# Kernel optimization log

Hardware: AMD Instinct MI355X
Metric: run time of the kernel (lower is better)

The kernel has to match this reference:

```python
import jax, jax.numpy as jnp
import numpy as np
import math

DIM = 1024
D_IN = 2048      # expand * dim
N = 16           # d_state
NG = 32          # ngroups
DT_RANK = 64     # ceil(dim/16)
D_CONV = 4
B, L = 2, 1024


def setup_inputs() -> dict:
    key = jax.random.key(0)
    ks = jax.random.split(key, 10)
    nrm = lambda k, shp, s: jax.random.normal(k, shp, jnp.float32) * s
    x = jax.random.normal(ks[0], (B, L, DIM), jnp.float32)
    latent = jnp.zeros((B, NG, D_IN, N), jnp.float32)
    W_in = nrm(ks[1], (2 * D_IN, DIM), 0.02)          # in_proj (no bias)
    conv_w = nrm(ks[2], (D_IN, 1, D_CONV), 0.1)        # depthwise conv weight
    conv_b = nrm(ks[3], (D_IN,), 0.02)                 # conv bias
    W_x = nrm(ks[4], (DT_RANK + 2 * N, D_IN), 0.02)    # x_proj (no bias)
    W_dt = nrm(ks[5], (D_IN, DT_RANK), 0.02)           # dt_proj weight
    b_dt = nrm(ks[6], (D_IN,), 0.1)                    # dt_proj bias
    W_out = nrm(ks[7], (DIM, D_IN), 0.02)              # out_proj (no bias)
    A_log = jnp.log(jnp.tile(jnp.arange(1, N + 1, dtype=jnp.float32), (D_IN, 1)))
    D = jnp.ones((D_IN,), jnp.float32)
    W_cattn = nrm(ks[8], (3 * N, N), 0.02)             # c_attn (no bias)
    return dict(x=x, latent=latent, W_in=W_in, conv_w=conv_w, conv_b=conv_b,
                W_x=W_x, W_dt=W_dt, b_dt=b_dt, W_out=W_out, A_log=A_log,
                D=D, W_cattn=W_cattn)


def _scan_op(e1, e2):
    a1, b1 = e1
    a2, b2 = e2
    return a2 * a1, a2 * b1 + b2


def reference(x, latent, W_in, conv_w, conv_b, W_x, W_dt, b_dt, W_out, A_log, D, W_cattn):
    b, l, _ = x.shape
    xr = x @ W_in.T                                  # [b,l,2*d_in]
    u, res = xr[..., :D_IN], xr[..., D_IN:]
    # depthwise causal conv1d (padding d_conv-1 then truncate to l == left-pad)
    uc = jnp.transpose(u, (0, 2, 1))                 # [b,d_in,l]
    uc = jax.lax.conv_general_dilated(
        uc, conv_w, window_strides=(1,), padding=[(D_CONV - 1, 0)],
        feature_group_count=D_IN, dimension_numbers=('NCH', 'OIH', 'NCH'))
    uc = uc + conv_b[None, :, None]
    u = jax.nn.silu(jnp.transpose(uc, (0, 2, 1)))    # [b,l,d_in]

    A = -jnp.exp(A_log)                              # [d_in,n]
    x_dbl = u @ W_x.T                                # [b,l,dt_rank+2n]
    delta = jax.nn.softplus(x_dbl[..., :DT_RANK] @ W_dt.T + b_dt)  # [b,l,d_in]
    Bm = x_dbl[..., DT_RANK:DT_RANK + N]             # [b,l,n]
    Cm = x_dbl[..., DT_RANK + N:]                    # [b,l,n]

    dA = jnp.exp(delta[..., None] * A)               # [b,l,d_in,n]
    dBu = delta[..., None] * Bm[:, :, None, :] * u[..., None]  # [b,l,d_in,n]

    pg = l // NG
    dA = dA.reshape(b, NG, pg, D_IN, N)
    dBu = dBu.reshape(b, NG, pg, D_IN, N)
    Cg = Cm.reshape(b, NG, pg, N)
    dBu = dBu.at[:, :, 0].add(latent)                # inject group latent

    # parallel scan of h_t = dA_t * h_{t-1} + dBu_t within each group
    _, hs = jax.lax.associative_scan(_scan_op, (dA, dBu), axis=2)
    y = jnp.einsum('bgpdn,bgpn->bgpd', hs, Cg).reshape(b, l, D_IN)
    y = y + u * D

    # latent communication: causal attention over group latents (initial latent, per source)
    qkv = latent[:, :-1] @ W_cattn.T                 # [b,ng-1,d_in,3n]
    q, k, v = jnp.split(qkv, 3, axis=-1)
    G = NG - 1
    q = q.reshape(b, G, -1)
    k = k.reshape(b, G, -1)
    v = v.reshape(b, G, -1)
    scale = 1.0 / math.sqrt(D_IN * N)
    scores = (q @ jnp.swapaxes(k, 1, 2)) * scale     # [b,G,G]
    mask = jnp.tril(jnp.ones((G, G), bool))
    scores = jnp.where(mask, scores, -jnp.inf)
    attn = jax.nn.softmax(scores, axis=-1)
    lat = (attn @ v).reshape(b, G, D_IN, N)
    lat_out = jnp.concatenate([jnp.zeros((b, 1, D_IN, N), x.dtype), lat], axis=1)

    out = (y * jax.nn.silu(res)) @ W_out.T           # [b,l,dim]
    return out, lat_out
```

## Files before the change

### kernel.cpp

```cpp
#include <hip/hip_runtime.h>
#include <stdint.h>

typedef uint16_t u16;
typedef u16   u16x4  __attribute__((ext_vector_type(4)));
typedef u16   u16x8  __attribute__((ext_vector_type(8)));
typedef __bf16 bf16x8 __attribute__((ext_vector_type(8)));
typedef float f32x4  __attribute__((ext_vector_type(4)));

__device__ __forceinline__ float b2f(u16 x) {
    union { uint32_t u; float f; } c; c.u = ((uint32_t)x) << 16; return c.f;
}
__device__ __forceinline__ u16 f2b(float f) {
    union { float f; uint32_t u; } c; c.f = f;
    uint32_t r = c.u + 0x7FFFu + ((c.u >> 16) & 1u);
    return (u16)(r >> 16);
}
__device__ __forceinline__ float silu_f(float x) { return x / (1.f + __expf(-x)); }

__device__ __forceinline__ void gload16(const u16* g, u16* l) {
    __builtin_amdgcn_global_load_lds(
        (const __attribute__((address_space(1))) void*)(g),
        (__attribute__((address_space(3))) void*)(l), 16, 0, 0);
}

__device__ __forceinline__ int dtype_flag_block(const u16* __restrict__ xraw) {
    __shared__ int bad;
    if (threadIdx.x == 0) bad = 0;
    __syncthreads();
    float v = b2f(xraw[threadIdx.x]);
    if (!(fabsf(v) < 1000.f)) atomicAdd(&bad, 1);
    __syncthreads();
    return bad;
}

struct CvtArgs {
    const void* s[14];
    u16* d[14];
    int cum[15];
    int total;
};
__global__ __launch_bounds__(256) void cvt_all_k(CvtArgs a, const u16* __restrict__ xraw)
{
    int flag = dtype_flag_block(xraw);
    int u4 = blockIdx.x * 256 + threadIdx.x;
    if (u4 >= a.total) return;
    int seg = 0;
    while (u4 >= a.cum[seg + 1]) seg++;
    int local = u4 - a.cum[seg];
    const void* s = a.s[seg];
    u16x4 o;
    if (s == nullptr) {
        o[0] = o[1] = o[2] = o[3] = 0;
    } else if (flag) {
        f32x4 vv = ((const f32x4*)s)[local];
        for (int e = 0; e < 4; e++) o[e] = f2b(vv[e]);
    } else {
        o = ((const u16x4*)s)[local];
    }
    *(u16x4*)(a.d[seg] + (size_t)local * 4) = o;
}

template<int EPI, int AF32>
__device__ __forceinline__ void gemm_core(
    int bx, int by, int bz,
    const u16* __restrict__ Ab, const float* __restrict__ Af,
    const u16* __restrict__ B,
    int Kc, int lda, int ldb,
    u16* __restrict__ Cb, float* __restrict__ Cf, int ldc, int ncols,
    const u16* __restrict__ bias, size_t zslab)
{
    __shared__ __align__(16) u16 lA[128 * 64];
    __shared__ __align__(16) u16 lB[128 * 64];
    const int tid  = threadIdx.x;
    const int wave = tid >> 6, lane = tid & 63;
    const int quad = lane >> 4, l16 = lane & 15;
    const int wm = wave & 1, wn = wave >> 1;
    const int row0 = by * 128, col0 = bx * 128;
    const int kbeg = bz * Kc;

    f32x4 acc[4][4];
    const f32x4 zf = {0.f, 0.f, 0.f, 0.f};
    for (int i = 0; i < 4; i++) for (int j = 0; j < 4; j++) acc[i][j] = zf;

    const u16* Abp[4]; const float* Afp[4]; const u16* Bp[4];
    int lbase[4], lofsA[4];
    for (int t = 0; t < 4; t++) {
        int c = t * 256 + tid;
        int r = c >> 3, s = c & 7;
        int q = (s - (r >> 1)) & 7;
        if (AF32) Afp[t] = Af + (size_t)(row0 + r) * lda + q * 8 + kbeg;
        else      Abp[t] = Ab + (size_t)(row0 + r) * lda + q * 8 + kbeg;
        Bp[t] = B + (size_t)(col0 + r) * ldb + q * 8 + kbeg;
        lbase[t] = (t * 256 + wave * 64) * 8;
        lofsA[t] = c * 8;
    }

    for (int k0 = 0; k0 < Kc; k0 += 64) {
        if (AF32) {
            for (int t = 0; t < 4; t++) {
                const float* ap = Afp[t] + k0;
                f32x4 v0 = *(const f32x4*)ap;
                f32x4 v1 = *(const f32x4*)(ap + 4);
                u16x8 w;
                for (int e = 0; e < 4; e++) { w[e] = f2b(v0[e]); w[4 + e] = f2b(v1[e]); }
                *(u16x8*)&lA[lofsA[t]] = w;
            }
        } else {
            for (int t = 0; t < 4; t++) gload16(Abp[t] + k0, &lA[lbase[t]]);
        }
        for (int t = 0; t < 4; t++) gload16(Bp[t] + k0, &lB[lbase[t]]);
        __syncthreads();
        for (int half = 0; half < 2; half++) {
            bf16x8 af[4], bfr[4];
            for (int i = 0; i < 4; i++) {
                int r = wm * 64 + i * 16 + l16;
                int s = (half * 4 + quad + (r >> 1)) & 7;
                af[i] = *(const bf16x8*)&lA[r * 64 + s * 8];
            }
            for (int j = 0; j < 4; j++) {
                int r = wn * 64 + j * 16 + l16;
                int s = (half * 4 + quad + (r >> 1)) & 7;
                bfr[j] = *(const bf16x8*)&lB[r * 64 + s * 8];
            }
            for (int i = 0; i < 4; i++)
                for (int j = 0; j < 4; j++)
                    acc[i][j] = __builtin_amdgcn_mfma_f32_16x16x32_bf16(af[i], bfr[j], acc[i][j], 0, 0, 0);
        }
        __syncthreads();
    }

    float* dstf = (EPI == 2) ? (Cf + (size_t)bz * zslab) : Cf;
    for (int i = 0; i < 4; i++) {
        int mb = row0 + wm * 64 + i * 16 + quad * 4;
        for (int j = 0; j < 4; j++) {
            int n = col0 + wn * 64 + j * 16 + l16;
            if (n >= ncols) continue;
            if (EPI == 0) {
                for (int v = 0; v < 4; v++)
                    Cb[(size_t)(mb + v) * ldc + n] = f2b(acc[i][j][v]);
            } else if (EPI == 1) {
                float bv = b2f(bias[n]);
                for (int v = 0; v < 4; v++) {
                    float xx = acc[i][j][v] + bv;
                    dstf[(size_t)(mb + v) * ldc + n] =
                        fmaxf(xx, 0.f) + log1pf(__expf(-fabsf(xx)));
                }
            } else if (EPI == 2) {
                for (int v = 0; v < 4; v++)
                    dstf[(size_t)(mb + v) * ldc + n] = acc[i][j][v];
            } else {
                for (int v = 0; v < 4; v++)
                    atomicAdd(&dstf[(size_t)(mb + v) * ldc + n], acc[i][j][v]);
            }
        }
    }
}

template<int EPI, int AF32>
__global__ __launch_bounds__(256) void gemm_bt(
    const u16* __restrict__ Ab, const float* __restrict__ Af,
    const u16* __restrict__ B, int Kc, int lda, int ldb,
    u16* __restrict__ Cb, float* __restrict__ Cf, int ldc, int ncols,
    const u16* __restrict__ bias, size_t zslab)
{
    gemm_core<EPI, AF32>(blockIdx.x, blockIdx.y, blockIdx.z,
                         Ab, Af, B, Kc, lda, ldb, Cb, Cf, ldc, ncols, bias, zslab);
}

__global__ __launch_bounds__(256) void conv_silu_k(
    const u16* __restrict__ xr, const u16* __restrict__ cw,
    const u16* __restrict__ cb, u16* __restrict__ u)
{
    int tid = threadIdx.x;
    int bl  = blockIdx.x;
    int l   = bl & 1023;
    int d0  = tid * 8;
    float acc[8];
    u16x8 bias = *(const u16x8*)&cb[d0];
    for (int j = 0; j < 8; j++) acc[j] = b2f(bias[j]);
    union { u16x8 v[4]; u16 s[32]; } wb;
    for (int t = 0; t < 4; t++) wb.v[t] = *(const u16x8*)&cw[d0 * 4 + t * 8];
    for (int t = 0; t < 4; t++) {
        int ls = l - 3 + t;
        if (ls < 0) continue;
        u16x8 xv = *(const u16x8*)&xr[(size_t)(bl - 3 + t) * 4096 + d0];
        for (int j = 0; j < 8; j++) acc[j] += b2f(xv[j]) * b2f(wb.s[j * 4 + t]);
    }
    u16x8 o;
    for (int j = 0; j < 8; j++) o[j] = f2b(silu_f(acc[j]));
    *(u16x8*)&u[(size_t)bl * 2048 + d0] = o;
}

__global__ __launch_bounds__(256) void scan_qkv_k(
    const float* __restrict__ delta, const u16* __restrict__ u,
    const u16* __restrict__ xr, const float* __restrict__ xf,
    const u16* __restrict__ latent, const u16* __restrict__ Alog,
    const u16* __restrict__ Dp, u16* __restrict__ yg,
    const u16* __restrict__ Wc, u16* __restrict__ q, u16* __restrict__ k,
    u16* __restrict__ v)
{
    __shared__ float sm[1024];
    int tid = threadIdx.x;
    int bid = blockIdx.x;
    if (bid < 512) {
        float (*Bs)[16] = (float(*)[16])sm;
        float (*Cs)[16] = (float(*)[16])(sm + 512);
        int dblk = bid & 7, bg = bid >> 3;
        int d = dblk * 256 + tid;
        for (int idx = tid; idx < 512; idx += 256) {
            int p = idx >> 4, n = idx & 15;
            const float* xp = &xf[(size_t)(bg * 32 + p) * 128];
            Bs[p][n] = xp[64 + n];
            Cs[p][n] = xp[80 + n];
        }
        __syncthreads();
        float a[16], h[16];
        {
            u16x8 a0 = *(const u16x8*)&Alog[(size_t)d * 16];
            u16x8 a1 = *(const u16x8*)&Alog[(size_t)d * 16 + 8];
            u16x8 l0 = *(const u16x8*)&latent[((size_t)bg * 2048 + d) * 16];
            u16x8 l1 = *(const u16x8*)&latent[((size_t)bg * 2048 + d) * 16 + 8];
            for (int n = 0; n < 8; n++) {
                a[n] = -__expf(b2f(a0[n])); a[8 + n] = -__expf(b2f(a1[n]));
                h[n] = b2f(l0[n]);          h[8 + n] = b2f(l1[n]);
            }
        }
        float Dd = b2f(Dp[d]);
        for (int p = 0; p < 32; p++) {
            size_t row = (size_t)bg * 32 + p;
            float dlt = delta[row * 2048 + d];
            float uu  = b2f(u[row * 2048 + d]);
            float db  = dlt * uu;
            float y = 0.f;
            if (p == 0) {
                for (int n = 0; n < 16; n++) { h[n] += db * Bs[0][n]; y += h[n] * Cs[0][n]; }
            } else {
                for (int n = 0; n < 16; n++) {
                    float w = __expf(dlt * a[n]);
                    h[n] = w * h[n] + db * Bs[p][n];
                    y += h[n] * Cs[p][n];
                }
            }
            float rs = b2f(xr[row * 4096 + 2048 + d]);
            yg[row * 2048 + d] = f2b((y + uu * Dd) * silu_f(rs));
        }
    } else {
        float (*Ws)[16] = (float(*)[16])sm;
        for (int i = tid; i < 768; i += 256) Ws[i >> 4][i & 15] = b2f(Wc[i]);
        __syncthreads();
        int gid = (bid - 512) * 256 + tid;
        int d = gid & 2047;
        int bi = gid >> 11;
        int b = bi / 31, i = bi - b * 31;
        const u16* lp = &latent[(((size_t)b * 32 + i) * 2048 + d) * 16];
        float lv[16];
        {
            u16x8 l0 = *(const u16x8*)lp, l1 = *(const u16x8*)(lp + 8);
            for (int m = 0; m < 8; m++) { lv[m] = b2f(l0[m]); lv[8 + m] = b2f(l1[m]); }
        }
        u16* outs[3] = {q, k, v};
        for (int pl = 0; pl < 3; pl++) {
            u16x8 o0, o1;
            for (int n = 0; n < 16; n++) {
                float s = 0.f;
                for (int m = 0; m < 16; m++) s += lv[m] * Ws[pl * 16 + n][m];
                if (n < 8) o0[n] = f2b(s); else o1[n - 8] = f2b(s);
            }
            u16* op = outs[pl] + (size_t)bi * 32768 + d * 16;
            *(u16x8*)op = o0; *(u16x8*)(op + 8) = o1;
        }
    }
}

__global__ __launch_bounds__(256) void gemm_scores_k(
    const u16* __restrict__ yg, const u16* __restrict__ Wout, float* __restrict__ out_part,
    const u16* __restrict__ q, const u16* __restrict__ kk, float* __restrict__ sc)
{
    int bid = blockIdx.x;
    if (bid < 512) {
        int bx = bid & 7, by = (bid >> 3) & 15, bz = bid >> 7;
        gemm_core<2, 0>(bx, by, bz, yg, nullptr, Wout, 512, 2048, 2048,
                        nullptr, out_part, 1024, 1024, nullptr, (size_t)2048 * 1024);
        return;
    }
    int idx = bid - 512;
    int b = idx / 961, r = idx - b * 961;
    int i = r / 31, j = r - i * 31;
    if (j > i) return;
    const u16* qp = q + ((size_t)b * 31 + i) * 32768;
    const u16* kp = kk + ((size_t)b * 31 + j) * 32768;
    float s = 0.f;
    for (int t = threadIdx.x * 8; t < 32768; t += 2048) {
        u16x8 a = *(const u16x8*)&qp[t];
        u16x8 c = *(const u16x8*)&kp[t];
        for (int e = 0; e < 8; e++) s += b2f(a[e]) * b2f(c[e]);
    }
    for (int off = 32; off; off >>= 1) s += __shfl_xor(s, off);
    __shared__ float red[4];
    if ((threadIdx.x & 63) == 0) red[threadIdx.x >> 6] = s;
    __syncthreads();
    if (threadIdx.x == 0)
        sc[idx] = (red[0] + red[1] + red[2] + red[3]) * 5.5242717e-3f;
}

__global__ __launch_bounds__(256) void attv_redout_k(
    const float* __restrict__ sc, const u16* __restrict__ v,
    const float* __restrict__ part, void* __restrict__ dout,
    const u16* __restrict__ xraw)
{
    int flag = dtype_flag_block(xraw);
    int bid = blockIdx.x;
    if (bid < 1024) {
        int chunk = bid & 15, bi = bid >> 4;
        int b = bi >> 5, i = (bi & 31) - 1;
        __shared__ float as[32];
        if (i >= 0 && threadIdx.x < 64) {
            float x = (threadIdx.x <= i) ? sc[(size_t)b * 961 + i * 31 + threadIdx.x] : -3.4e38f;
            float mx = x;
            for (int off = 32; off; off >>= 1) mx = fmaxf(mx, __shfl_xor(mx, off));
            float e = (threadIdx.x <= i) ? __expf(x - mx) : 0.f;
            float sm = e;
            for (int off = 32; off; off >>= 1) sm += __shfl_xor(sm, off);
            if (threadIdx.x < 32) as[threadIdx.x] = e / sm;
        }
        __syncthreads();
        int dn = chunk * 2048 + threadIdx.x * 8;
        float acc[8] = {0, 0, 0, 0, 0, 0, 0, 0};
        if (i >= 0) {
            for (int j = 0; j <= i; j++) {
                u16x8 vv = *(const u16x8*)&v[((size_t)b * 31 + j) * 32768 + dn];
                float aj = as[j];
                for (int e = 0; e < 8; e++) acc[e] += aj * b2f(vv[e]);
            }
            for (int e = 0; e < 8; e++) if (!(fabsf(acc[e]) < 1e30f)) acc[e] = 0.f;
        }
        size_t ofs = 2097152 + ((size_t)b * 32 + (i + 1)) * 32768 + dn;
        if (flag) {
            f32x4 o0, o1;
            for (int e = 0; e < 4; e++) { o0[e] = acc[e]; o1[e] = acc[4 + e]; }
            *(f32x4*)((float*)dout + ofs) = o0;
            *(f32x4*)((float*)dout + ofs + 4) = o1;
        } else {
            u16x8 o;
            for (int e = 0; e < 8; e++) o[e] = f2b(acc[e]);
            *(u16x8*)((u16*)dout + ofs) = o;
        }
    } else {
        int gid = (bid - 1024) * 256 + threadIdx.x;
        int m = gid >> 8;
        int j = (gid & 255) * 4;
        f32x4 s = {0.f, 0.f, 0.f, 0.f};
        for (int ks = 0; ks < 4; ks++) {
            f32x4 p = *(const f32x4*)&part[((size_t)ks * 2048 + m) * 1024 + j];
            for (int e = 0; e < 4; e++) s[e] += p[e];
        }
        for (int e = 0; e < 4; e++) if (!(fabsf(s[e]) < 1e30f)) s[e] = 0.f;
        if (flag) {
            ((f32x4*)dout)[(size_t)m * 256 + (j >> 2)] = s;
        } else {
            u16x4 o;
            for (int e = 0; e < 4; e++) o[e] = f2b(s[e]);
            ((u16x4*)dout)[(size_t)m * 256 + (j >> 2)] = o;
        }
    }
}

extern "C" void kernel_launch(void* const* d_in, const int* in_sizes, int n_in,
                              void* d_out, int out_size, void* d_ws, size_t ws_size,
                              hipStream_t stream)
{
    char* ws = (char*)d_ws;
    const u16* xraw = (const u16*)d_in[0];
    u16* cx    = (u16*)(ws + 0);
    u16* clat  = (u16*)(ws + 4194304);
    u16* cWin  = (u16*)(ws + 8388608);
    u16* ccw   = (u16*)(ws + 16777216);
    u16* ccb   = (u16*)(ws + 16793600);
    u16* wxp   = (u16*)(ws + 16797696);
    u16* cWdt  = (u16*)(ws + 17321984);
    u16* cbdt  = (u16*)(ws + 17584128);
    u16* cWout = (u16*)(ws + 17588224);
    u16* cAlog = (u16*)(ws + 21782528);
    u16* cD    = (u16*)(ws + 21848064);
    u16* cWc   = (u16*)(ws + 21852160);
    float* xdbl_f32 = (float*)(ws + 21853760);
    float* sc       = (float*)(ws + 22902336);
    u16*   u        = (u16*)(ws + 22910080);
    u16*   xr       = (u16*)(ws + 31298688);
    u16*   yg       = (u16*)(ws + 48075904);
    float* delta    = (float*)(ws + 56464512);
    u16*   qb       = (u16*)(ws + 73241728);
    u16*   kb       = qb + 2031616;
    u16*   vb       = kb + 2031616;
    float* out_part = (float*)(ws + 85431424);

    CvtArgs ca;
    const void* srcs[14] = { d_in[0], d_in[1], d_in[2], d_in[3], d_in[4],
                             d_in[5], nullptr, d_in[6], d_in[7], d_in[8],
                             d_in[9], d_in[10], d_in[11], nullptr };
    u16* dsts[14] = { cx, clat, cWin, ccw, ccb,
                      wxp, wxp + 196608, cWdt, cbdt, cWout,
                      cAlog, cD, cWc, (u16*)xdbl_f32 };
    int ns[14] = { 2097152, 2097152, 4194304, 8192, 2048,
                   196608, 65536, 131072, 2048, 2097152,
                   32768, 2048, 768, 524288 };
    int cum = 0;
    for (int i = 0; i < 14; i++) {
        ca.s[i] = srcs[i]; ca.d[i] = dsts[i];
        ca.cum[i] = cum; cum += ns[i] / 4;
    }
    ca.cum[14] = cum; ca.total = cum;
    cvt_all_k<<<(cum + 255) / 256, 256, 0, stream>>>(ca, xraw);

    gemm_bt<0, 0><<<dim3(32, 16, 1), 256, 0, stream>>>(cx, nullptr, cWin, 1024, 1024, 1024,
                                                       xr, nullptr, 4096, 4096, nullptr, 0);
    conv_silu_k<<<2048, 256, 0, stream>>>(xr, ccw, ccb, u);
    gemm_bt<3, 0><<<dim3(1, 16, 16), 256, 0, stream>>>(u, nullptr, wxp, 128, 2048, 2048,
                                                       nullptr, xdbl_f32, 128, 128, nullptr, 0);
    gemm_bt<1, 1><<<dim3(16, 16, 1), 256, 0, stream>>>(nullptr, xdbl_f32, cWdt, 64, 128, 64,
                                                       nullptr, delta, 2048, 2048, cbdt, 0);
    scan_qkv_k<<<1008, 256, 0, stream>>>(delta, u, xr, xdbl_f32, clat, cAlog, cD, yg,
                                         cWc, qb, kb, vb);
    gemm_scores_k<<<2434, 256, 0, stream>>>(yg, cWout, out_part, qb, kb, sc);
    attv_redout_k<<<3072, 256, 0, stream>>>(sc, vb, out_part, d_out, xraw);
}
```

Before: 261.4 us.

## Replace x_proj atomics with split-K partial slabs and retile GEMMs to 64-wide N

The x_proj split-K GEMM now writes 16 separate fp32 partial slabs instead of using atomicAdd into a zeroed buffer. The dt_proj GEMM and the scan kernel sum those slabs on load, which also removes the zero-fill segment from the convert kernel. The GEMM template gains a TN parameter: in_proj and out_proj use 128x64 tiles to launch more blocks, and out_proj halves its split-K from 4 to 2 with the reduction adjusted to match. This trades atomic contention for extra reads of the partial slabs and more workspace memory.

New measurement: 257.6 us. Within noise of the previous version (-1.5%).

```diff
diff --git a/kernel.cpp b/kernel.cpp
--- a/kernel.cpp
+++ b/kernel.cpp
@@ -34,9 +34,9 @@
 }
 
 struct CvtArgs {
-    const void* s[14];
-    u16* d[14];
-    int cum[15];
+    const void* s[13];
+    u16* d[13];
+    int cum[14];
     int total;
 };
 __global__ __launch_bounds__(256) void cvt_all_k(CvtArgs a, const u16* __restrict__ xraw)
@@ -60,7 +60,7 @@
     *(u16x4*)(a.d[seg] + (size_t)local * 4) = o;
 }
 
-template<int EPI, int AF32>
+template<int EPI, int AMODE, int TN>
 __device__ __forceinline__ void gemm_core(
     int bx, int by, int bz,
     const u16* __restrict__ Ab, const float* __restrict__ Af,
@@ -69,61 +69,74 @@
     u16* __restrict__ Cb, float* __restrict__ Cf, int ldc, int ncols,
     const u16* __restrict__ bias, size_t zslab)
 {
+    constexpr int NJ = TN / 32;
+    constexpr int BT = TN / 32;
     __shared__ __align__(16) u16 lA[128 * 64];
-    __shared__ __align__(16) u16 lB[128 * 64];
+    __shared__ __align__(16) u16 lB[TN * 64];
     const int tid  = threadIdx.x;
     const int wave = tid >> 6, lane = tid & 63;
     const int quad = lane >> 4, l16 = lane & 15;
     const int wm = wave & 1, wn = wave >> 1;
-    const int row0 = by * 128, col0 = bx * 128;
+    const int row0 = by * 128, col0 = bx * TN;
     const int kbeg = bz * Kc;
 
-    f32x4 acc[4][4];
+    f32x4 acc[4][NJ];
     const f32x4 zf = {0.f, 0.f, 0.f, 0.f};
-    for (int i = 0; i < 4; i++) for (int j = 0; j < 4; j++) acc[i][j] = zf;
-
-    const u16* Abp[4]; const float* Afp[4]; const u16* Bp[4];
-    int lbase[4], lofsA[4];
+    for (int i = 0; i < 4; i++) for (int j = 0; j < NJ; j++) acc[i][j] = zf;
+
+    const u16* Abp[4]; const float* Afp[4]; const u16* Bp[BT];
+    int lbaseA[4], lofsA[4], lbaseB[BT];
     for (int t = 0; t < 4; t++) {
         int c = t * 256 + tid;
         int r = c >> 3, s = c & 7;
         int q = (s - (r >> 1)) & 7;
-        if (AF32) Afp[t] = Af + (size_t)(row0 + r) * lda + q * 8 + kbeg;
-        else      Abp[t] = Ab + (size_t)(row0 + r) * lda + q * 8 + kbeg;
+        if (AMODE == 2) Afp[t] = Af + (size_t)(row0 + r) * lda + q * 8 + kbeg;
+        else            Abp[t] = Ab + (size_t)(row0 + r) * lda + q * 8 + kbeg;
+        lbaseA[t] = (t * 256 + wave * 64) * 8;
+        lofsA[t] = c * 8;
+    }
+    for (int t = 0; t < BT; t++) {
+        int c = t * 256 + tid;
+        int r = c >> 3, s = c & 7;
+        int q = (s - (r >> 1)) & 7;
         Bp[t] = B + (size_t)(col0 + r) * ldb + q * 8 + kbeg;
-        lbase[t] = (t * 256 + wave * 64) * 8;
-        lofsA[t] = c * 8;
+        lbaseB[t] = (t * 256 + wave * 64) * 8;
     }
 
     for (int k0 = 0; k0 < Kc; k0 += 64) {
-        if (AF32) {
+        if (AMODE == 2) {
             for (int t = 0; t < 4; t++) {
                 const float* ap = Afp[t] + k0;
-                f32x4 v0 = *(const f32x4*)ap;
-                f32x4 v1 = *(const f32x4*)(ap + 4);
+                float v[8];
+                for (int e = 0; e < 8; e++) v[e] = 0.f;
+                for (int s = 0; s < 16; s++) {
+                    f32x4 v0 = *(const f32x4*)(ap + (size_t)s * 262144);
+                    f32x4 v1 = *(const f32x4*)(ap + (size_t)s * 262144 + 4);
+                    for (int e = 0; e < 4; e++) { v[e] += v0[e]; v[4 + e] += v1[e]; }
+                }
                 u16x8 w;
-                for (int e = 0; e < 4; e++) { w[e] = f2b(v0[e]); w[4 + e] = f2b(v1[e]); }
+                for (int e = 0; e < 8; e++) w[e] = f2b(v[e]);
                 *(u16x8*)&lA[lofsA[t]] = w;
             }
         } else {
-            for (int t = 0; t < 4; t++) gload16(Abp[t] + k0, &lA[lbase[t]]);
-        }
-        for (int t = 0; t < 4; t++) gload16(Bp[t] + k0, &lB[lbase[t]]);
+            for (int t = 0; t < 4; t++) gload16(Abp[t] + k0, &lA[lbaseA[t]]);
+        }
+        for (int t = 0; t < BT; t++) gload16(Bp[t] + k0, &lB[lbaseB[t]]);
         __syncthreads();
         for (int half = 0; half < 2; half++) {
-            bf16x8 af[4], bfr[4];
+            bf16x8 af[4], bfr[NJ];
             for (int i = 0; i < 4; i++) {
                 int r = wm * 64 + i * 16 + l16;
                 int s = (half * 4 + quad + (r >> 1)) & 7;
                 af[i] = *(const bf16x8*)&lA[r * 64 + s * 8];
             }
-            for (int j = 0; j < 4; j++) {
-                int r = wn * 64 + j * 16 + l16;
+            for (int j = 0; j < NJ; j++) {
+                int r = wn * (TN / 2) + j * 16 + l16;
                 int s = (half * 4 + quad + (r >> 1)) & 7;
                 bfr[j] = *(const bf16x8*)&lB[r * 64 + s * 8];
             }
             for (int i = 0; i < 4; i++)
-                for (int j = 0; j < 4; j++)
+                for (int j = 0; j < NJ; j++)
                     acc[i][j] = __builtin_amdgcn_mfma_f32_16x16x32_bf16(af[i], bfr[j], acc[i][j], 0, 0, 0);
         }
         __syncthreads();
@@ -132,8 +145,8 @@
     float* dstf = (EPI == 2) ? (Cf + (size_t)bz * zslab) : Cf;
     for (int i = 0; i < 4; i++) {
         int mb = row0 + wm * 64 + i * 16 + quad * 4;
-        for (int j = 0; j < 4; j++) {
-            int n = col0 + wn * 64 + j * 16 + l16;
+        for (int j = 0; j < NJ; j++) {
+            int n = col0 + wn * (TN / 2) + j * 16 + l16;
             if (n >= ncols) continue;
             if (EPI == 0) {
                 for (int v = 0; v < 4; v++)
@@ -145,26 +158,23 @@
                     dstf[(size_t)(mb + v) * ldc + n] =
                         fmaxf(xx, 0.f) + log1pf(__expf(-fabsf(xx)));
                 }
-            } else if (EPI == 2) {
+            } else {
                 for (int v = 0; v < 4; v++)
                     dstf[(size_t)(mb + v) * ldc + n] = acc[i][j][v];
-            } else {
-                for (int v = 0; v < 4; v++)
-                    atomicAdd(&dstf[(size_t)(mb + v) * ldc + n], acc[i][j][v]);
-            }
-        }
-    }
-}
-
-template<int EPI, int AF32>
+            }
+        }
+    }
+}
+
+template<int EPI, int AMODE, int TN>
 __global__ __launch_bounds__(256) void gemm_bt(
     const u16* __restrict__ Ab, const float* __restrict__ Af,
     const u16* __restrict__ B, int Kc, int lda, int ldb,
     u16* __restrict__ Cb, float* __restrict__ Cf, int ldc, int ncols,
     const u16* __restrict__ bias, size_t zslab)
 {
-    gemm_core<EPI, AF32>(blockIdx.x, blockIdx.y, blockIdx.z,
-                         Ab, Af, B, Kc, lda, ldb, Cb, Cf, ldc, ncols, bias, zslab);
+    gemm_core<EPI, AMODE, TN>(blockIdx.x, blockIdx.y, blockIdx.z,
+                              Ab, Af, B, Kc, lda, ldb, Cb, Cf, ldc, ncols, bias, zslab);
 }
 
 __global__ __launch_bounds__(256) void conv_silu_k(
@@ -193,7 +203,7 @@
 
 __global__ __launch_bounds__(256) void scan_qkv_k(
     const float* __restrict__ delta, const u16* __restrict__ u,
-    const u16* __restrict__ xr, const float* __restrict__ xf,
+    const u16* __restrict__ xr, const float* __restrict__ xpart,
     const u16* __restrict__ latent, const u16* __restrict__ Alog,
     const u16* __restrict__ Dp, u16* __restrict__ yg,
     const u16* __restrict__ Wc, u16* __restrict__ q, u16* __restrict__ k,
@@ -207,11 +217,13 @@
         float (*Cs)[16] = (float(*)[16])(sm + 512);
         int dblk = bid & 7, bg = bid >> 3;
         int d = dblk * 256 + tid;
-        for (int idx = tid; idx < 512; idx += 256) {
-            int p = idx >> 4, n = idx & 15;
-            const float* xp = &xf[(size_t)(bg * 32 + p) * 128];
-            Bs[p][n] = xp[64 + n];
-            Cs[p][n] = xp[80 + n];
+        for (int idx = tid; idx < 1024; idx += 256) {
+            int p = (idx >> 4) & 31, n = idx & 15;
+            int which = idx >> 9;
+            const float* xp = &xpart[(size_t)(bg * 32 + p) * 128 + 64 + which * 16 + n];
+            float s = 0.f;
+            for (int sl = 0; sl < 16; sl++) s += xp[(size_t)sl * 262144];
+            if (which == 0) Bs[p][n] = s; else Cs[p][n] = s;
         }
         __syncthreads();
         float a[16], h[16];
@@ -278,9 +290,9 @@
 {
     int bid = blockIdx.x;
     if (bid < 512) {
-        int bx = bid & 7, by = (bid >> 3) & 15, bz = bid >> 7;
-        gemm_core<2, 0>(bx, by, bz, yg, nullptr, Wout, 512, 2048, 2048,
-                        nullptr, out_part, 1024, 1024, nullptr, (size_t)2048 * 1024);
+        int bx = bid & 15, by = (bid >> 4) & 15, bz = bid >> 8;
+        gemm_core<2, 0, 64>(bx, by, bz, yg, nullptr, Wout, 1024, 2048, 2048,
+                            nullptr, out_part, 1024, 1024, nullptr, (size_t)2048 * 1024);
         return;
     }
     int idx = bid - 512;
@@ -350,7 +362,7 @@
         int m = gid >> 8;
         int j = (gid & 255) * 4;
         f32x4 s = {0.f, 0.f, 0.f, 0.f};
-        for (int ks = 0; ks < 4; ks++) {
+        for (int ks = 0; ks < 2; ks++) {
             f32x4 p = *(const f32x4*)&part[((size_t)ks * 2048 + m) * 1024 + j];
             for (int e = 0; e < 4; e++) s[e] += p[e];
         }
@@ -383,43 +395,44 @@
     u16* cAlog = (u16*)(ws + 21782528);
     u16* cD    = (u16*)(ws + 21848064);
     u16* cWc   = (u16*)(ws + 21852160);
-    float* xdbl_f32 = (float*)(ws + 21853760);
-    float* sc       = (float*)(ws + 22902336);
-    u16*   u        = (u16*)(ws + 22910080);
-    u16*   xr       = (u16*)(ws + 31298688);
-    u16*   yg       = (u16*)(ws + 48075904);
-    float* delta    = (float*)(ws + 56464512);
-    u16*   qb       = (u16*)(ws + 73241728);
-    u16*   kb       = qb + 2031616;
-    u16*   vb       = kb + 2031616;
-    float* out_part = (float*)(ws + 85431424);
+    float* xdbl_part = (float*)(ws + 21853760);
+    float* sc        = (float*)(ws + 38630976);
+    u16*   u         = (u16*)(ws + 38638720);
+    u16*   xr        = (u16*)(ws + 47027328);
+    u16*   yg        = (u16*)(ws + 63804544);
+    float* delta     = (float*)(ws + 72193152);
+    u16*   qb        = (u16*)(ws + 88970368);
+    u16*   kb        = qb + 2031616;
+    u16*   vb        = kb + 2031616;
+    float* out_part  = (float*)(ws + 101160064);
 
     CvtArgs ca;
-    const void* srcs[14] = { d_in[0], d_in[1], d_in[2], d_in[3], d_in[4],
+    const void* srcs[13] = { d_in[0], d_in[1], d_in[2], d_in[3], d_in[4],
                              d_in[5], nullptr, d_in[6], d_in[7], d_in[8],
-                             d_in[9], d_in[10], d_in[11], nullptr };
-    u16* dsts[14] = { cx, clat, cWin, ccw, ccb,
+                             d_in[9], d_in[10], d_in[11] };
+    u16* dsts[13] = { cx, clat, cWin, ccw, ccb,
                       wxp, wxp + 196608, cWdt, cbdt, cWout,
-                      cAlog, cD, cWc, (u16*)xdbl_f32 };
-    int ns[14] = { 2097152, 2097152, 4194304, 8192, 2048,
+                      cAlog, cD, cWc };
+    int ns[13] = { 2097152, 2097152, 4194304, 8192, 2048,
                    196608, 65536, 131072, 2048, 2097152,
-                   32768, 2048, 768, 524288 };
+                   32768, 2048, 768 };
     int cum = 0;
-    for (int i = 0; i < 14; i++) {
+    for (int i = 0; i < 13; i++) {
         ca.s[i] = srcs[i]; ca.d[i] = dsts[i];
         ca.cum[i] = cum; cum += ns[i] / 4;
     }
-    ca.cum[14] = cum; ca.total = cum;
+    ca.cum[13] = cum; ca.total = cum;
     cvt_all_k<<<(cum + 255) / 256, 256, 0, stream>>>(ca, xraw);
 
-    gemm_bt<0, 0><<<dim3(32, 16, 1), 256, 0, stream>>>(cx, nullptr, cWin, 1024, 1024, 1024,
-                                                       xr, nullptr, 4096, 4096, nullptr, 0);
+    gemm_bt<0, 0, 64><<<dim3(64, 16, 1), 256, 0, stream>>>(cx, nullptr, cWin, 1024, 1024, 1024,
+                                                           xr, nullptr, 4096, 4096, nullptr, 0);
     conv_silu_k<<<2048, 256, 0, stream>>>(xr, ccw, ccb, u);
-    gemm_bt<3, 0><<<dim3(1, 16, 16), 256, 0, stream>>>(u, nullptr, wxp, 128, 2048, 2048,
-                                                       nullptr, xdbl_f32, 128, 128, nullptr, 0);
-    gemm_bt<1, 1><<<dim3(16, 16, 1), 256, 0, stream>>>(nullptr, xdbl_f32, cWdt, 64, 128, 64,
-                                                       nullptr, delta, 2048, 2048, cbdt, 0);
-    scan_qkv_k<<<1008, 256, 0, stream>>>(delta, u, xr, xdbl_f32, clat, cAlog, cD, yg,
+    gemm_bt<2, 0, 128><<<dim3(1, 16, 16), 256, 0, stream>>>(u, nullptr, wxp, 128, 2048, 2048,
+                                                            nullptr, xdbl_part, 128, 128,
+                                                            nullptr, 262144);
+    gemm_bt<1, 2, 128><<<dim3(16, 16, 1), 256, 0, stream>>>(nullptr, xdbl_part, cWdt, 64, 128, 64,
+                                                            nullptr, delta, 2048, 2048, cbdt, 0);
+    scan_qkv_k<<<1008, 256, 0, stream>>>(delta, u, xr, xdbl_part, clat, cAlog, cD, yg,
                                          cWc, qb, kb, vb);
     gemm_scores_k<<<2434, 256, 0, stream>>>(yg, cWout, out_part, qb, kb, sc);
     attv_redout_k<<<3072, 256, 0, stream>>>(sc, vb, out_part, d_out, xraw);
```
